# Kernel optimization log

Measured on AMD Instinct MI355X. Metric: run time of the kernel, lower is better.

The kernel has to match this reference:

```python
import jax, jax.numpy as jnp
import numpy as np

NUM_HEADS = 3

def setup_inputs() -> dict:
    key = jax.random.key(0)
    k0, k1, k2, k3, k4 = jax.random.split(key, 5)
    B, C, H, W = 2, 96, 64, 64
    N = H * W
    x = jax.random.normal(k0, (B, N, C), jnp.float32)
    # depthwise conv: groups=C, out_channels=3*C -> OIHW weight [3C, 1, 3, 3]
    qkv_w = jax.random.normal(k1, (3 * C, 1, 3, 3), jnp.float32) * 0.1
    qkv_b = jax.random.normal(k2, (3 * C,), jnp.float32) * 0.01
    proj_w = jax.random.normal(k3, (C, C), jnp.float32) * (1.0 / np.sqrt(C))
    proj_b = jax.random.normal(k4, (C,), jnp.float32) * 0.01
    return {"x": x, "qkv_w": qkv_w, "qkv_b": qkv_b,
            "proj_w": proj_w, "proj_b": proj_b, "H": H, "W": W}


def reference(x, qkv_w, qkv_b, proj_w, proj_b, H, W):
    B, N, C = x.shape
    h = NUM_HEADS
    d = C // h
    scale = d ** (-0.5)
    # [B,N,C] -> [B,C,H,W]
    x2d = jnp.transpose(x, (0, 2, 1)).reshape(B, C, H, W)
    # depthwise conv, 'SAME' padding (padding = kernel//2, stride 1)
    qkv = jax.lax.conv_general_dilated(
        x2d, qkv_w, window_strides=(1, 1), padding="SAME",
        feature_group_count=C,
        dimension_numbers=("NCHW", "OIHW", "NCHW"))
    qkv = qkv + qkv_b[None, :, None, None]
    qkv = qkv.reshape(B, 3, h, d, H * W)  # same channel split as torch reshape
    q, k, v = qkv[:, 0], qkv[:, 1], qkv[:, 2]  # each [B,h,d,N]
    # attn = q^T @ k  (q,k permuted to [B,h,N,d] in the original)
    attn = jnp.einsum("bhdn,bhdm->bhnm", q, k) * scale  # [B,h,N,N]
    attn = jax.nn.softmax(attn, axis=-1)
    out = jnp.einsum("bhnm,bhdm->bhnd", attn, v)  # [B,h,N,d]
    # replicate torch: transpose(2,3) -> [B,h,d,N], reshape(B, N, C)
    out = jnp.transpose(out, (0, 1, 3, 2)).reshape(B, H * W, C)
    out = out @ proj_w.T + proj_b
    return out
```

## Files before the change

### kernel.cpp

```cpp
#include <hip/hip_runtime.h>
#include <hip/hip_bf16.h>

typedef short bf16x8 __attribute__((ext_vector_type(8)));
typedef float f32x4 __attribute__((ext_vector_type(4)));
typedef unsigned int u32x4 __attribute__((ext_vector_type(4)));

#define B_ 2
#define C_ 96
#define N_ 4096
#define NH_ 3
#define DH_ 32
#define BH_ 6
#define KSPLIT 2
#define TQ 64
#define MQ 4
#define TK 64
#define WAVES_PER_BLOCK 4
#define KT_PER_WAVE (N_ / KSPLIT / WAVES_PER_BLOCK / TK)


__global__ __launch_bounds__(256) void conv_qkv(
    const float* __restrict__ x, const float* __restrict__ qw,
    const float* __restrict__ qb, __hip_bfloat16* __restrict__ q_b,
    __hip_bfloat16* __restrict__ k_b, __hip_bfloat16* __restrict__ vT) {
  __shared__ float xs[18 * 64];
  int b = blockIdx.x / C_;
  int cin = blockIdx.x % C_;
  int y0 = blockIdx.y * 16;
  int yl0 = (y0 == 0) ? 0 : y0 - 1;
  int yl1 = (y0 + 16 > 63) ? 63 : y0 + 16;
  int nload = (yl1 - yl0 + 1) * 64;
  const float* xp = x + (size_t)b * N_ * C_ + cin;
  for (int i = threadIdx.x; i < nload; i += 256)
    xs[i] = xp[(size_t)(yl0 * 64 + i) * C_];
  __syncthreads();

  int s = cin >> 5;
  int cl = cin & 31;
  float w[3][9], bias[3];
#pragma unroll
  for (int r = 0; r < 3; ++r) {
    int o = 3 * cin + r;
#pragma unroll
    for (int t = 0; t < 9; ++t) w[r][t] = qw[o * 9 + t];
    bias[r] = qb[o];
  }
  const float scale = 0.2550349f;
  float mul = (s == 0) ? scale : 1.0f;
  __hip_bfloat16* base_[3];
  int dd_[3];
#pragma unroll
  for (int r = 0; r < 3; ++r) {
    int c = 3 * cl + r, head = c >> 5, dd = c & 31, bh = b * NH_ + head;
    dd_[r] = dd;
    if (s == 2)
      base_[r] = vT + (size_t)bh * N_ * DH_;
    else if (s == 1)
      base_[r] = k_b + (size_t)bh * N_ * DH_;
    else
      base_[r] = q_b + (size_t)bh * N_ * DH_;
  }

  for (int i = threadIdx.x; i < 1024; i += 256) {
    int y = y0 + (i >> 6), xx = i & 63;
    float a0 = bias[0], a1 = bias[1], a2 = bias[2];
#pragma unroll
    for (int dy = 0; dy < 3; ++dy) {
      int ry = y + dy - 1;
      if ((unsigned)ry >= 64u) continue;
#pragma unroll
      for (int dx = 0; dx < 3; ++dx) {
        int rx = xx + dx - 1;
        if ((unsigned)rx >= 64u) continue;
        float xv = xs[(ry - yl0) * 64 + rx];
        a0 += w[0][dy * 3 + dx] * xv;
        a1 += w[1][dy * 3 + dx] * xv;
        a2 += w[2][dy * 3 + dx] * xv;
      }
    }
    int n = y * 64 + xx;
    float av[3] = {a0 * mul, a1 * mul, a2 * mul};
#pragma unroll
    for (int r = 0; r < 3; ++r) {
      int off;
      if (s == 0)
        off = n * DH_ + dd_[r];
      else if (s == 1)
        off = ((n >> 6) << 11) | (((n >> 4) & 3) << 9) | ((n & 15) << 5) | dd_[r];
      else {
        int kap = (((n >> 2) & 3) << 3) | (((n >> 4) & 1) << 2) | (n & 3);
        off = ((n >> 6) << 11) | (((n >> 5) & 1) << 10) | (dd_[r] << 5) | kap;
      }
      base_[r][off] = __float2bfloat16(av[r]);
    }
  }
}

__global__ __launch_bounds__(256, 2) void attn_fwd(
    const __hip_bfloat16* __restrict__ q_b, const __hip_bfloat16* __restrict__ k_b,
    const __hip_bfloat16* __restrict__ vT, float* __restrict__ Opart,
    float* __restrict__ lpart) {
  __shared__ __align__(16) float Tm[WAVES_PER_BLOCK][32 * 65];
  __shared__ float l_s[WAVES_PER_BLOCK][TQ];
  int qt = blockIdx.x, ks = blockIdx.y, bh = blockIdx.z;
  int tid = threadIdx.x;
  int lane = tid & 63, wave = tid >> 6;
  int c = lane & 15, quad = lane >> 4;

  const __hip_bfloat16* qbase = q_b + ((size_t)bh * N_ + qt * TQ) * DH_;
  bf16x8 qa[MQ];
#pragma unroll
  for (int m = 0; m < MQ; ++m)
    qa[m] = *(const bf16x8*)(qbase + (m * 16 + c) * DH_ + quad * 8);

  f32x4 oT[2][MQ];
  f32x4 lacT[MQ];
#pragma unroll
  for (int m = 0; m < MQ; ++m) {
    lacT[m] = (f32x4){0.f, 0.f, 0.f, 0.f};
#pragma unroll
    for (int n0 = 0; n0 < 2; ++n0) oT[n0][m] = (f32x4){0.f, 0.f, 0.f, 0.f};
  }
  bf16x8 ones;
  {
    short v = (c == 0) ? (short)0x3F80 : (short)0;
    ones = (bf16x8){v, v, v, v, v, v, v, v};
  }

  const __hip_bfloat16* kb = k_b + (size_t)bh * N_ * DH_;
  const __hip_bfloat16* vb = vT + (size_t)bh * N_ * DH_;
  int key0 = ks * (N_ / KSPLIT) + wave * (N_ / KSPLIT / WAVES_PER_BLOCK);

  bf16x8 kf[2][4];
  bf16x8 vf[2][2][2];
  {
    size_t tb0 = (size_t)key0 * DH_;
#pragma unroll
    for (int t = 0; t < 4; ++t)
      kf[0][t] = *(const bf16x8*)(kb + tb0 + t * 512 + c * 32 + quad * 8);
#pragma unroll
    for (int n0 = 0; n0 < 2; ++n0)
#pragma unroll
      for (int h = 0; h < 2; ++h)
        vf[0][n0][h] = *(const bf16x8*)(vb + tb0 + h * 1024 + (n0 * 16 + c) * 32 + quad * 8);
  }

#pragma unroll
  for (int kt = 0; kt < KT_PER_WAVE; ++kt) {
    const int cur = kt & 1, nxt = cur ^ 1;

    if (kt + 1 < KT_PER_WAVE) {
      size_t tnext = (size_t)(key0 + (kt + 1) * TK) * DH_;
#pragma unroll
      for (int t = 0; t < 4; ++t)
        kf[nxt][t] = *(const bf16x8*)(kb + tnext + t * 512 + c * 32 + quad * 8);
#pragma unroll
      for (int n0 = 0; n0 < 2; ++n0)
#pragma unroll
        for (int h = 0; h < 2; ++h)
          vf[nxt][n0][h] = *(const bf16x8*)(vb + tnext + h * 1024 + (n0 * 16 + c) * 32 + quad * 8);
    }

#pragma unroll
    for (int m = 0; m < MQ; ++m) {
      f32x4 pT[4];
      f32x4 z = {0.f, 0.f, 0.f, 0.f};
#pragma unroll
      for (int t = 0; t < 4; ++t)
        pT[t] = __builtin_amdgcn_mfma_f32_16x16x32_bf16(kf[cur][t], qa[m], z, 0, 0, 0);

#pragma unroll
      for (int t = 0; t < 4; ++t)
#pragma unroll
        for (int r = 0; r < 4; ++r)
          pT[t][r] = __builtin_amdgcn_exp2f(pT[t][r]);

      unsigned wv[4][2];
#pragma unroll
      for (int t = 0; t < 4; ++t) {
        unsigned h0 = __builtin_bit_cast(unsigned short, __float2bfloat16(pT[t][0]));
        unsigned h1 = __builtin_bit_cast(unsigned short, __float2bfloat16(pT[t][1]));
        unsigned h2 = __builtin_bit_cast(unsigned short, __float2bfloat16(pT[t][2]));
        unsigned h3 = __builtin_bit_cast(unsigned short, __float2bfloat16(pT[t][3]));
        wv[t][0] = h0 | (h1 << 16);
        wv[t][1] = h2 | (h3 << 16);
      }
#pragma unroll
      for (int h = 0; h < 2; ++h) {
        u32x4 bw = {wv[2 * h][0], wv[2 * h][1], wv[2 * h + 1][0], wv[2 * h + 1][1]};
        bf16x8 pB = __builtin_bit_cast(bf16x8, bw);
        oT[0][m] = __builtin_amdgcn_mfma_f32_16x16x32_bf16(vf[cur][0][h], pB, oT[0][m], 0, 0, 0);
        oT[1][m] = __builtin_amdgcn_mfma_f32_16x16x32_bf16(vf[cur][1][h], pB, oT[1][m], 0, 0, 0);
        lacT[m] = __builtin_amdgcn_mfma_f32_16x16x32_bf16(ones, pB, lacT[m], 0, 0, 0);
      }
    }
  }

  float* T = Tm[wave];
#pragma unroll
  for (int n0 = 0; n0 < 2; ++n0)
#pragma unroll
    for (int m = 0; m < MQ; ++m)
#pragma unroll
      for (int r = 0; r < 4; ++r)
        T[(n0 * 16 + quad * 4 + r) * 65 + m * 16 + c] = oT[n0][m][r];
  if (lane < 16) {
#pragma unroll
    for (int m = 0; m < MQ; ++m) l_s[wave][m * 16 + lane] = lacT[m][0];
  }
  __syncthreads();

  int nbase = qt * TQ;
  float* Ob = Opart + (size_t)(ks * BH_ + bh) * DH_ * N_ + nbase;
  const float* Sf = (const float*)Tm;
#pragma unroll
  for (int it = 0; it < 8; ++it) {
    int idx = it * 256 + tid;
    int dd = idx >> 6, q = idx & 63;
    float s = Sf[0 * 2080 + dd * 65 + q] + Sf[1 * 2080 + dd * 65 + q] +
              Sf[2 * 2080 + dd * 65 + q] + Sf[3 * 2080 + dd * 65 + q];
    Ob[(size_t)dd * N_ + q] = s;
  }
  if (tid < TQ) {
    float s = l_s[0][tid] + l_s[1][tid] + l_s[2][tid] + l_s[3][tid];
    lpart[(size_t)(ks * BH_ + bh) * N_ + nbase + tid] = s;
  }
}

__global__ __launch_bounds__(256) void proj_out(
    const float* __restrict__ Opart, const float* __restrict__ lpart,
    const float* __restrict__ pw, const float* __restrict__ pb,
    float* __restrict__ out) {
  __shared__ float Wt[C_][100];
  __shared__ float Pt[16][100];
  __shared__ float bias[C_];
  int tid = threadIdx.x;
  for (int i = tid; i < C_ * C_; i += 256) Wt[i / C_][i % C_] = pw[i];
  if (tid < C_) bias[tid] = pb[tid];
  int row0 = blockIdx.x * 16;
  for (int i = tid; i < 16 * C_; i += 256) {
    int r = i / C_, cc = i % C_;
    int g = row0 + r;
    int b = g >> 12;
    int f = (g & 4095) * C_ + cc;
    int hh = f >> 17;
    int n = f & 4095;
    float osum = 0.f, lsum = 0.f;
    size_t obase = (size_t)g * C_ + cc;
    size_t lbase = (size_t)(b * NH_ + hh) * N_ + n;
#pragma unroll
    for (int ksq = 0; ksq < KSPLIT; ++ksq) {
      osum += Opart[(size_t)ksq * (BH_ * DH_ * N_) + obase];
      lsum += lpart[(size_t)ksq * (BH_ * N_) + lbase];
    }
    Pt[r][cc] = osum / lsum;
  }
  __syncthreads();

  int row = tid >> 4, cg = tid & 15;
  float acc[6] = {};
  for (int kk = 0; kk < C_; kk += 4) {
    f32x4 pv = *(const f32x4*)&Pt[row][kk];
    f32x4 wv[6];
#pragma unroll
    for (int i2 = 0; i2 < 6; ++i2) wv[i2] = *(const f32x4*)&Wt[cg * 6 + i2][kk];
#pragma unroll
    for (int i2 = 0; i2 < 6; ++i2)
      acc[i2] += pv[0] * wv[i2][0] + pv[1] * wv[i2][1] +
                 pv[2] * wv[i2][2] + pv[3] * wv[i2][3];
  }
#pragma unroll
  for (int i2 = 0; i2 < 6; ++i2)
    out[(size_t)(row0 + row) * C_ + cg * 6 + i2] = acc[i2] + bias[cg * 6 + i2];
}

extern "C" void kernel_launch(void* const* d_in, const int* in_sizes, int n_in,
                              void* d_out, int out_size, void* d_ws, size_t ws_size,
                              hipStream_t stream) {
  const float* x = (const float*)d_in[0];
  const float* qw = (const float*)d_in[1];
  const float* qb = (const float*)d_in[2];
  const float* pw = (const float*)d_in[3];
  const float* pb = (const float*)d_in[4];

  char* ws = (char*)d_ws;
  __hip_bfloat16* q_b = (__hip_bfloat16*)(ws);
  __hip_bfloat16* k_b = (__hip_bfloat16*)(ws + 1572864);
  __hip_bfloat16* vT = (__hip_bfloat16*)(ws + 3145728);
  float* Opart = (float*)(ws + 4718592);
  float* lpart = (float*)(ws + 11010048);

  hipLaunchKernelGGL(conv_qkv, dim3(B_ * C_, 4), dim3(256), 0, stream, x, qw, qb, q_b, k_b, vT);
  hipLaunchKernelGGL(attn_fwd, dim3(N_ / TQ, KSPLIT, BH_), dim3(256), 0, stream,
                     q_b, k_b, vT, Opart, lpart);
  hipLaunchKernelGGL(proj_out, dim3((B_ * N_) / 16, 1), dim3(256), 0, stream,
                     Opart, lpart, pw, pb, (float*)d_out);
}
```

Measured before the change: 117.4 us.

## Tile depthwise conv over 8 channels with padded shared halo for coalesced loads

Result: faster. 109.7 us (-6.5%).

```diff
diff --git a/kernel.cpp b/kernel.cpp
--- a/kernel.cpp
+++ b/kernel.cpp
@@ -17,24 +17,38 @@
 #define TK 64
 #define WAVES_PER_BLOCK 4
 #define KT_PER_WAVE (N_ / KSPLIT / WAVES_PER_BLOCK / TK)
+#define CHB 8
+#define CROWS 4
 
 
 __global__ __launch_bounds__(256) void conv_qkv(
     const float* __restrict__ x, const float* __restrict__ qw,
     const float* __restrict__ qb, __hip_bfloat16* __restrict__ q_b,
     __hip_bfloat16* __restrict__ k_b, __hip_bfloat16* __restrict__ vT) {
-  __shared__ float xs[18 * 64];
-  int b = blockIdx.x / C_;
-  int cin = blockIdx.x % C_;
-  int y0 = blockIdx.y * 16;
-  int yl0 = (y0 == 0) ? 0 : y0 - 1;
-  int yl1 = (y0 + 16 > 63) ? 63 : y0 + 16;
-  int nload = (yl1 - yl0 + 1) * 64;
-  const float* xp = x + (size_t)b * N_ * C_ + cin;
-  for (int i = threadIdx.x; i < nload; i += 256)
-    xs[i] = xp[(size_t)(yl0 * 64 + i) * C_];
+  __shared__ float xs[6][66][CHB];
+  int b = blockIdx.x / 12;
+  int chg = blockIdx.x % 12;
+  int ch0 = chg * CHB;
+  int y0 = blockIdx.y * CROWS;
+  int t = threadIdx.x;
+
+  if (t < 96) {
+    int lr = t >> 4, side = (t >> 3) & 1, ch = t & 7;
+    xs[lr][side ? 65 : 0][ch] = 0.f;
+  }
+  const float* xb = x + (size_t)b * N_ * C_ + ch0;
+  for (int i = t; i < 6 * 64 * CHB; i += 256) {
+    int lr = i >> 9;
+    int rem = i & 511;
+    int col = rem >> 3, ch = rem & 7;
+    int gy = y0 - 1 + lr;
+    float v = 0.f;
+    if ((unsigned)gy < 64u) v = xb[(size_t)(gy * 64 + col) * C_ + ch];
+    xs[lr][col + 1][ch] = v;
+  }
   __syncthreads();
 
+  int cin = ch0 + (t & 7);
   int s = cin >> 5;
   int cl = cin & 31;
   float w[3][9], bias[3];
@@ -42,7 +56,7 @@
   for (int r = 0; r < 3; ++r) {
     int o = 3 * cin + r;
 #pragma unroll
-    for (int t = 0; t < 9; ++t) w[r][t] = qw[o * 9 + t];
+    for (int tap = 0; tap < 9; ++tap) w[r][tap] = qw[o * 9 + tap];
     bias[r] = qb[o];
   }
   const float scale = 0.2550349f;
@@ -61,24 +75,22 @@
       base_[r] = q_b + (size_t)bh * N_ * DH_;
   }
 
-  for (int i = threadIdx.x; i < 1024; i += 256) {
-    int y = y0 + (i >> 6), xx = i & 63;
+  int pslot = t >> 3, chl = t & 7;
+#pragma unroll
+  for (int pr = 0; pr < 8; ++pr) {
+    int pos = pr * 32 + pslot;
+    int y = pos >> 6, xcol = pos & 63;
     float a0 = bias[0], a1 = bias[1], a2 = bias[2];
 #pragma unroll
-    for (int dy = 0; dy < 3; ++dy) {
-      int ry = y + dy - 1;
-      if ((unsigned)ry >= 64u) continue;
+    for (int dy = 0; dy < 3; ++dy)
 #pragma unroll
       for (int dx = 0; dx < 3; ++dx) {
-        int rx = xx + dx - 1;
-        if ((unsigned)rx >= 64u) continue;
-        float xv = xs[(ry - yl0) * 64 + rx];
+        float xv = xs[y + dy][xcol + dx][chl];
         a0 += w[0][dy * 3 + dx] * xv;
         a1 += w[1][dy * 3 + dx] * xv;
         a2 += w[2][dy * 3 + dx] * xv;
       }
-    }
-    int n = y * 64 + xx;
+    int n = (y0 + y) * 64 + xcol;
     float av[3] = {a0 * mul, a1 * mul, a2 * mul};
 #pragma unroll
     for (int r = 0; r < 3; ++r) {
@@ -290,7 +302,7 @@
   float* Opart = (float*)(ws + 4718592);
   float* lpart = (float*)(ws + 11010048);
 
-  hipLaunchKernelGGL(conv_qkv, dim3(B_ * C_, 4), dim3(256), 0, stream, x, qw, qb, q_b, k_b, vT);
+  hipLaunchKernelGGL(conv_qkv, dim3(B_ * 12, 16), dim3(256), 0, stream, x, qw, qb, q_b, k_b, vT);
   hipLaunchKernelGGL(attn_fwd, dim3(N_ / TQ, KSPLIT, BH_), dim3(256), 0, stream,
                      q_b, k_b, vT, Opart, lpart);
   hipLaunchKernelGGL(proj_out, dim3((B_ * N_) / 16, 1), dim3(256), 0, stream,
```
